# Performance work log

Measured on AMD Instinct MI355X. Metric: run time of the kernel, lower is better.

Reference implementation:

```python
import jax, jax.numpy as jnp
import numpy as np

NUM_HEADS = 16


def setup_inputs() -> dict:
    key = jax.random.key(0)
    ks = jax.random.split(key, 5)
    S, B, N, C = 4, 2, 2048, 1024
    return {
        "x_all": jax.random.normal(ks[0], (S, B, N, C), dtype=jnp.float32),
        "w_qkv": jax.random.normal(ks[1], (C, 3 * C), dtype=jnp.float32) * (C ** -0.5),
        "b_qkv": jax.random.normal(ks[2], (3 * C,), dtype=jnp.float32) * 0.02,
        "w_proj": jax.random.normal(ks[3], (C, C), dtype=jnp.float32) * (C ** -0.5),
        "b_proj": jax.random.normal(ks[4], (C,), dtype=jnp.float32) * 0.02,
    }


def reference(x_all, w_qkv, b_qkv, w_proj, b_proj):
    # x_all: [S, B, N, C] -- S = cp_dim ring shards, each rank holds [B, N, C]
    S, B, N, C = x_all.shape
    H = NUM_HEADS
    D = C // H
    scale = 1.0 / np.sqrt(D).astype(np.float32)

    # same qkv projection on every rank
    qkv = (jnp.einsum("sbnc,ce->sbne", x_all, w_qkv) + b_qkv)
    qkv = qkv.reshape(S, B, N, 3, H, D)
    # rank 0's queries: [B, H, N, D]
    q = jnp.transpose(qkv[0, :, :, 0], (0, 2, 1, 3))
    # all shards' keys/values: [S, B, H, N, D]
    k = jnp.transpose(qkv[:, :, :, 1], (0, 1, 3, 2, 4))
    v = jnp.transpose(qkv[:, :, :, 2], (0, 1, 3, 2, 4))

    # ring loop: online softmax merge across KV shards (numerically stable
    # form of the source's exp(lse)-weighted average)
    attn_out, lse = None, None
    for s in range(S):
        scores = jnp.einsum("bhnd,bhmd->bhnm", q, k[s]) * scale  # [B,H,N,N]
        new_lse = jax.nn.logsumexp(scores, axis=-1)               # [B,H,N]
        probs = jnp.exp(scores - new_lse[..., None])
        new_out = jnp.einsum("bhnm,bhmd->bhnd", probs, v[s])      # [B,H,N,D]
        if attn_out is None:
            attn_out, lse = new_out, new_lse
        else:
            m = jnp.logaddexp(lse, new_lse)
            attn_out = (attn_out * jnp.exp(lse - m)[..., None]
                        + new_out * jnp.exp(new_lse - m)[..., None])
            lse = m

    # [B,H,N,D] -> [B,N,C]
    out = jnp.transpose(attn_out, (0, 2, 1, 3)).reshape(B, N, C)
    return out @ w_proj + b_proj
```

## Files before the change

kernel.cpp:

```cpp
#include <hip/hip_runtime.h>
#include <hip/hip_bf16.h>


typedef __bf16 bf16x8 __attribute__((ext_vector_type(8)));
typedef float v4f __attribute__((ext_vector_type(4)));

#if __has_builtin(__builtin_amdgcn_exp2f)
#define EXP2F(x) __builtin_amdgcn_exp2f(x)
#else
#define EXP2F(x) exp2f(x)
#endif

__device__ __forceinline__ float bf2f(unsigned short h) {
  union { unsigned int u; float f; } a; a.u = ((unsigned int)h) << 16; return a.f;
}
__device__ __forceinline__ unsigned short f2bf(float f) {
  union { float f; unsigned int u; } a; a.f = f;
  unsigned int u = a.u;
  unsigned int r = (u + 0x7fffu + ((u >> 16) & 1u)) >> 16;
  return (unsigned short)r;
}
__device__ __forceinline__ unsigned int pack2t(float a, float b) {
  union { float f; unsigned int u; } ua, ub; ua.f = a; ub.f = b;
#if __has_builtin(__builtin_amdgcn_perm)
  return __builtin_amdgcn_perm(ub.u, ua.u, 0x07060302u);
#else
  return (ua.u >> 16) | (ub.u & 0xffff0000u);
#endif
}
__device__ __forceinline__ bf16x8 ldfrag16(const unsigned short* p) {
  union { uint4 u; bf16x8 v; } x; x.u = *(const uint4*)p; return x.v;
}
__device__ __forceinline__ bf16x8 ones8() {
  union { unsigned short s[8]; bf16x8 v; } x;
#pragma unroll
  for (int i = 0; i < 8; i++) x.s[i] = 0x3F80;
  return x.v;
}
__device__ __forceinline__ void gld_lds16(const unsigned short* g, unsigned short* l) {
  __builtin_amdgcn_global_load_lds((__attribute__((address_space(1))) void*)g,
                                   (__attribute__((address_space(3))) void*)l, 16, 0, 0);
}

__global__ void detect_dtype(const unsigned short* __restrict__ x, int* flag) {
  __shared__ int cnt;
  if (threadIdx.x == 0) cnt = 0;
  __syncthreads();
  int sane = 0;
#pragma unroll
  for (int j = 0; j < 4; j++) {
    unsigned short v = x[2 * (threadIdx.x + 64 * j)];
    int e = (v >> 7) & 0xFF;
    if (e >= 90 && e <= 140) sane++;
  }
  atomicAdd(&cnt, sane);
  __syncthreads();
  if (threadIdx.x == 0) *flag = (cnt > 160) ? 0 : 1;
}

__global__ void conv_to_bf16(const void* __restrict__ in, unsigned short* __restrict__ out,
                             int n4, const int* __restrict__ flag) {
  int i = blockIdx.x * blockDim.x + threadIdx.x;
  if (i >= n4) return;
  if (*flag) {
    float4 v = ((const float4*)in)[i];
    ushort4 o;
    o.x = f2bf(v.x); o.y = f2bf(v.y); o.z = f2bf(v.z); o.w = f2bf(v.w);
    ((ushort4*)out)[i] = o;
  } else {
    ((ushort4*)out)[i] = ((const ushort4*)in)[i];
  }
}

__global__ void conv_bias(const void* __restrict__ bq_in, const void* __restrict__ bp_in,
                          unsigned short* __restrict__ bq, unsigned short* __restrict__ bp,
                          const int* __restrict__ flag) {
  int i = blockIdx.x * 256 + threadIdx.x;
  const void* in = (i < 768) ? bq_in : bp_in;
  unsigned short* out = (i < 768) ? bq : bp;
  int j = (i < 768) ? i : i - 768;
  if (*flag) {
    float4 v = ((const float4*)in)[j];
    ushort4 o;
    o.x = f2bf(v.x); o.y = f2bf(v.y); o.z = f2bf(v.z); o.w = f2bf(v.w);
    ((ushort4*)out)[j] = o;
  } else {
    ((ushort4*)out)[j] = ((const ushort4*)in)[j];
  }
}

__global__ void trans_both(const void* __restrict__ wqkv, const void* __restrict__ wproj,
                           unsigned short* __restrict__ wt1, unsigned short* __restrict__ wt2,
                           const int* __restrict__ flag) {
  __shared__ unsigned short t[32][33];
  int tx = threadIdx.x, ty = threadIdx.y;
  int bx = blockIdx.x;
  const void* in; unsigned short* out; int C, c0;
  if (bx < 96) { in = wqkv; out = wt1; C = 3072; c0 = bx * 32; }
  else         { in = wproj; out = wt2; C = 1024; c0 = (bx - 96) * 32; }
  const int R = 1024;
  int r0 = blockIdx.y * 32;
  int fp = *flag;
#pragma unroll
  for (int j = 0; j < 32; j += 8) {
    unsigned short v;
    if (fp) v = f2bf(((const float*)in)[(r0 + ty + j) * C + c0 + tx]);
    else    v = ((const unsigned short*)in)[(r0 + ty + j) * C + c0 + tx];
    t[ty + j][tx] = v;
  }
  __syncthreads();
#pragma unroll
  for (int j = 0; j < 32; j += 8) out[(c0 + ty + j) * R + r0 + tx] = t[tx][ty + j];
}

template <int MODE>
__launch_bounds__(256, 3)
__global__ void gemm_bt(const unsigned short* __restrict__ A,
                        const unsigned short* __restrict__ Bt,
                        const unsigned short* __restrict__ bias,
                        void* __restrict__ Cout,
                        int K, int ldc, const int* __restrict__ flag,
                        const unsigned short* Bt2, const unsigned short* bias2,
                        void* Cout2,
                        const unsigned short* Bt3, const unsigned short* bias3,
                        void* Cout3) {
  __shared__ unsigned short As[128 * 64];
  __shared__ unsigned short Bs[128 * 64];
  int tid = threadIdx.x;
  int w = tid >> 6, lane = tid & 63, col = lane & 15, quad = lane >> 4;
  int wm = w >> 1, wn = w & 1;
  const unsigned short* Bt_ = Bt;
  const unsigned short* bias_ = bias;
  void* Cout_ = Cout;
  bool isq = false, isv = false;
  int n0, m0;
  if constexpr (MODE == 4) {
    int id = blockIdx.x;
    int xcd = id & 7, t = id >> 3;
    n0 = (t & 7) * 128;
    int y = xcd * 36 + (t >> 3);
    if (y < 256) {
      m0 = (y >> 1) * 128;
      if (y & 1) { isv = true; Bt_ = Bt3; bias_ = bias3; Cout_ = Cout3; }
    } else {
      m0 = (y - 256) * 128;
      isq = true; Bt_ = Bt2; bias_ = bias2; Cout_ = Cout2;
    }
  } else {
    int id = blockIdx.x;
    int xcd = id & 7, t = id >> 3;
    n0 = (t & 7) * 128;
    m0 = (xcd * 4 + (t >> 3)) * 128;
  }
  int fp = 0;
  if constexpr (MODE == 2) fp = *flag;

  v4f acc[4][4];
#pragma unroll
  for (int i = 0; i < 4; i++)
#pragma unroll
    for (int j = 0; j < 4; j++) acc[i][j] = v4f{0.f, 0.f, 0.f, 0.f};

  int row0 = tid >> 3, c0 = tid & 7;
  int sw = c0;
  int cg0 = (sw ^ (row0 & 7)) * 8;
  const unsigned short* ga0 = &A[(m0 + row0) * K + cg0];
  const unsigned short* ga1 = ga0 + 32 * K;
  const unsigned short* ga2 = ga0 + 64 * K;
  const unsigned short* ga3 = ga0 + 96 * K;
  const unsigned short* gb0 = &Bt_[(n0 + row0) * K + cg0];
  const unsigned short* gb1 = gb0 + 32 * K;
  const unsigned short* gb2 = gb0 + 64 * K;
  const unsigned short* gb3 = gb0 + 96 * K;
  unsigned short* lA0 = &As[w * 512];
  unsigned short* lA1 = &As[2048 + w * 512];
  unsigned short* lA2 = &As[4096 + w * 512];
  unsigned short* lA3 = &As[6144 + w * 512];
  unsigned short* lB0 = &Bs[w * 512];
  unsigned short* lB1 = &Bs[2048 + w * 512];
  unsigned short* lB2 = &Bs[4096 + w * 512];
  unsigned short* lB3 = &Bs[6144 + w * 512];

  int niter = K >> 6;
  for (int it = 0; it < niter; it++) {
    __syncthreads();
    gld_lds16(ga0, lA0); gld_lds16(ga1, lA1);
    gld_lds16(ga2, lA2); gld_lds16(ga3, lA3);
    gld_lds16(gb0, lB0); gld_lds16(gb1, lB1);
    gld_lds16(gb2, lB2); gld_lds16(gb3, lB3);
    ga0 += 64; ga1 += 64; ga2 += 64; ga3 += 64;
    gb0 += 64; gb1 += 64; gb2 += 64; gb3 += 64;
    __syncthreads();
#pragma unroll
    for (int kk = 0; kk < 2; kk++) {
      bf16x8 af[4], bfr[4];
#pragma unroll
      for (int mi = 0; mi < 4; mi++) {
        int row = wm * 64 + mi * 16 + col;
        af[mi] = ldfrag16(&As[row * 64 + 8 * ((kk * 4 + quad) ^ (col & 7))]);
      }
#pragma unroll
      for (int ni = 0; ni < 4; ni++) {
        int row = wn * 64 + ni * 16 + col;
        bfr[ni] = ldfrag16(&Bs[row * 64 + 8 * ((kk * 4 + quad) ^ (col & 7))]);
      }
#pragma unroll
      for (int mi = 0; mi < 4; mi++)
#pragma unroll
        for (int ni = 0; ni < 4; ni++)
          acc[mi][ni] = __builtin_amdgcn_mfma_f32_16x16x32_bf16(af[mi], bfr[ni], acc[mi][ni], 0, 0, 0);
    }
  }

  float bv[4];
#pragma unroll
  for (int ni = 0; ni < 4; ni++) bv[ni] = bf2f(bias_[n0 + wn * 64 + ni * 16 + col]);

  if (MODE == 4 && isv) {
    int rgb0 = m0 + wm * 64;
    int s = rgb0 >> 12, b = (rgb0 >> 11) & 1, n = rgb0 & 2047;
    int kvg0 = s * 2048 + n;
#pragma unroll
    for (int ni = 0; ni < 4; ni++) {
      int cg = n0 + wn * 64 + ni * 16 + col;
      int h = cg >> 6, d = cg & 63;
      unsigned short* rowp = &((unsigned short*)Cout_)[((b * 16 + h) * 64 + d) * 8192 + kvg0];
      float bvn = bv[ni];
#pragma unroll
      for (int r = 0; r < 4; r++) {
        ushort2 e, o2;
        e.x = f2bf(acc[0][ni][r] + bvn);
        e.y = f2bf(acc[2][ni][r] + bvn);
        o2.x = f2bf(acc[1][ni][r] + bvn);
        o2.y = f2bf(acc[3][ni][r] + bvn);
        *(ushort2*)&rowp[2 * (quad * 4 + r)] = e;
        *(ushort2*)&rowp[32 + 2 * (quad * 4 + r)] = o2;
      }
    }
  } else {
#pragma unroll
    for (int mi = 0; mi < 4; mi++)
#pragma unroll
      for (int ni = 0; ni < 4; ni++) {
        float vals[4];
#pragma unroll
        for (int r = 0; r < 4; r++) vals[r] = acc[mi][ni][r] + bv[ni];
        if constexpr (MODE == 4) {
          if (isq) {
#pragma unroll
            for (int r = 0; r < 4; r++) vals[r] *= 0.1803368801111601f;
          }
        }
        int rgb = m0 + wm * 64 + mi * 16 + quad * 4;
        int cg  = n0 + wn * 64 + ni * 16 + col;
        if constexpr (MODE == 4) {
          unsigned short* C = (unsigned short*)Cout_;
#pragma unroll
          for (int r = 0; r < 4; r++) C[(rgb + r) * ldc + cg] = f2bf(vals[r]);
        } else {
          if (fp) {
            float* C = (float*)Cout_;
#pragma unroll
            for (int r = 0; r < 4; r++) C[(rgb + r) * ldc + cg] = vals[r];
          } else {
            unsigned short* C = (unsigned short*)Cout_;
#pragma unroll
            for (int r = 0; r < 4; r++) C[(rgb + r) * ldc + cg] = f2bf(vals[r]);
          }
        }
      }
  }
}

__launch_bounds__(512, 4)
__global__ void attn_kernel(const unsigned short* __restrict__ qbuf,
                            const unsigned short* __restrict__ kbuf,
                            const unsigned short* __restrict__ vt,
                            float* __restrict__ po,
                            float* __restrict__ lbuf) {
  __shared__ unsigned short Ks[2][64 * 64];
  __shared__ unsigned short Vs[3][64 * 64];
  int tid = threadIdx.x;
  int w = tid >> 6, lane = tid & 63, col = lane & 15, quad = lane >> 4;
  int id = blockIdx.x;
  int xcd = id & 7, slot = id >> 3;
  int qt = slot & 7, gsub = slot >> 3;
  int g = gsub * 8 + xcd;
  int bh = g >> 1, half = g & 1;
  int b = bh >> 4, h = bh & 15;
  int q0 = qt * 256;

  bf16x8 aQ[2][2];
#pragma unroll
  for (int mj = 0; mj < 2; mj++)
#pragma unroll
    for (int kk = 0; kk < 2; kk++)
      aQ[mj][kk] = ldfrag16(&qbuf[(b * 2048 + q0 + w * 32 + mj * 16 + col) * 1024 +
                                  h * 64 + kk * 32 + quad * 8]);

  int r0 = tid >> 3, c0 = tid & 7;
  const unsigned short* kp = &kbuf[((half * 2) * 4096 + b * 2048 + r0) * 1024 + h * 64 + c0 * 8];
  const unsigned short* vp = &vt[(bh * 64 + r0) * 8192 + half * 4096 + c0 * 8];
  int sdst = r0 * 64 + 8 * (c0 ^ (r0 & 7));

  const bf16x8 vone = ones8();
  v4f o[2][4];
  v4f acc_l[2] = {v4f{0.f, 0.f, 0.f, 0.f}, v4f{0.f, 0.f, 0.f, 0.f}};
#pragma unroll
  for (int mj = 0; mj < 2; mj++)
#pragma unroll
    for (int di = 0; di < 4; di++) o[mj][di] = v4f{0.f, 0.f, 0.f, 0.f};

  {
    uint4 k0 = *(const uint4*)kp, v0 = *(const uint4*)vp;
    *(uint4*)&Ks[0][sdst] = k0;
    *(uint4*)&Vs[0][sdst] = v0;
  }
  kp += 64 * 1024; vp += 64;
  uint4 pk = *(const uint4*)kp, pv = *(const uint4*)vp;
  __syncthreads();

  bf16x8 aP[2][2];
  {
    v4f sc[4][2];
#pragma unroll
    for (int ni = 0; ni < 4; ni++)
#pragma unroll
      for (int mj = 0; mj < 2; mj++) sc[ni][mj] = v4f{0.f, 0.f, 0.f, 0.f};
#pragma unroll
    for (int kk = 0; kk < 2; kk++) {
      bf16x8 aK[4];
#pragma unroll
      for (int ni = 0; ni < 4; ni++) {
        int row = ni * 16 + col;
        aK[ni] = ldfrag16(&Ks[0][row * 64 + 8 * ((kk * 4 + quad) ^ (col & 7))]);
      }
#pragma unroll
      for (int ni = 0; ni < 4; ni++)
#pragma unroll
        for (int mj = 0; mj < 2; mj++)
          sc[ni][mj] = __builtin_amdgcn_mfma_f32_16x16x32_bf16(aK[ni], aQ[mj][kk], sc[ni][mj], 0, 0, 0);
    }
#pragma unroll
    for (int ni = 0; ni < 4; ni++)
#pragma unroll
      for (int mj = 0; mj < 2; mj++)
#pragma unroll
        for (int r = 0; r < 4; r++) sc[ni][mj][r] = EXP2F(sc[ni][mj][r]);
#pragma unroll
    for (int mj = 0; mj < 2; mj++)
#pragma unroll
      for (int kk = 0; kk < 2; kk++) {
        union { unsigned int d[4]; bf16x8 v; } u;
#pragma unroll
        for (int t = 0; t < 4; t++)
          u.d[t] = pack2t(sc[kk][mj][t], sc[kk + 2][mj][t]);
        aP[mj][kk] = u.v;
      }
  }
  *(uint4*)&Ks[1][sdst] = pk;
  *(uint4*)&Vs[1][sdst] = pv;
  __syncthreads();

  const unsigned short* vprev = Vs[0];
  const unsigned short* vcur  = Vs[1];
  const unsigned short* vnext = Vs[2];

  for (int t = 1; t < 64; t++) {
    const unsigned short* kcur = Ks[t & 1];
    unsigned short* knxt = (unsigned short*)Ks[(t + 1) & 1];
    if (t < 63) {
      int kstep = (((t + 1) & 31) == 0) ? (2048 + 64) * 1024 : 64 * 1024;
      kp += kstep; vp += 64;
      pk = *(const uint4*)kp; pv = *(const uint4*)vp;
    }

    v4f sc[4][2];
#pragma unroll
    for (int ni = 0; ni < 4; ni++)
#pragma unroll
      for (int mj = 0; mj < 2; mj++) sc[ni][mj] = v4f{0.f, 0.f, 0.f, 0.f};
#pragma unroll
    for (int kk = 0; kk < 2; kk++) {
      bf16x8 aK[4];
#pragma unroll
      for (int ni = 0; ni < 4; ni++) {
        int row = ni * 16 + col;
        aK[ni] = ldfrag16(&kcur[row * 64 + 8 * ((kk * 4 + quad) ^ (col & 7))]);
      }
#pragma unroll
      for (int ni = 0; ni < 4; ni++)
#pragma unroll
        for (int mj = 0; mj < 2; mj++)
          sc[ni][mj] = __builtin_amdgcn_mfma_f32_16x16x32_bf16(aK[ni], aQ[mj][kk], sc[ni][mj], 0, 0, 0);
    }

#pragma unroll
    for (int kk = 0; kk < 2; kk++) {
#pragma unroll
      for (int mj = 0; mj < 2; mj++)
        acc_l[mj] = __builtin_amdgcn_mfma_f32_16x16x32_bf16(aP[mj][kk], vone, acc_l[mj], 0, 0, 0);
      bf16x8 bV[4];
#pragma unroll
      for (int di = 0; di < 4; di++) {
        int row = di * 16 + col;
        bV[di] = ldfrag16(&vprev[row * 64 + 8 * ((kk * 4 + quad) ^ (col & 7))]);
      }
#pragma unroll
      for (int mj = 0; mj < 2; mj++)
#pragma unroll
        for (int di = 0; di < 4; di++)
          o[mj][di] = __builtin_amdgcn_mfma_f32_16x16x32_bf16(aP[mj][kk], bV[di], o[mj][di], 0, 0, 0);
    }

#pragma unroll
    for (int ni = 0; ni < 4; ni++)
#pragma unroll
      for (int mj = 0; mj < 2; mj++)
#pragma unroll
        for (int r = 0; r < 4; r++) sc[ni][mj][r] = EXP2F(sc[ni][mj][r]);
    bf16x8 aPn[2][2];
#pragma unroll
    for (int mj = 0; mj < 2; mj++)
#pragma unroll
      for (int kk = 0; kk < 2; kk++) {
        union { unsigned int d[4]; bf16x8 v; } u;
#pragma unroll
        for (int tt = 0; tt < 4; tt++)
          u.d[tt] = pack2t(sc[kk][mj][tt], sc[kk + 2][mj][tt]);
        aPn[mj][kk] = u.v;
      }

    if (t < 63) {
      *(uint4*)&knxt[sdst] = pk;
      *(uint4*)&((unsigned short*)vnext)[sdst] = pv;
    }

    __syncthreads();

#pragma unroll
    for (int mj = 0; mj < 2; mj++)
#pragma unroll
      for (int kk = 0; kk < 2; kk++) aP[mj][kk] = aPn[mj][kk];
    const unsigned short* vt_ = vprev;
    vprev = vcur; vcur = vnext; vnext = vt_;
  }

#pragma unroll
  for (int kk = 0; kk < 2; kk++) {
#pragma unroll
    for (int mj = 0; mj < 2; mj++)
      acc_l[mj] = __builtin_amdgcn_mfma_f32_16x16x32_bf16(aP[mj][kk], vone, acc_l[mj], 0, 0, 0);
    bf16x8 bV[4];
#pragma unroll
    for (int di = 0; di < 4; di++) {
      int row = di * 16 + col;
      bV[di] = ldfrag16(&vprev[row * 64 + 8 * ((kk * 4 + quad) ^ (col & 7))]);
    }
#pragma unroll
    for (int mj = 0; mj < 2; mj++)
#pragma unroll
      for (int di = 0; di < 4; di++)
        o[mj][di] = __builtin_amdgcn_mfma_f32_16x16x32_bf16(aP[mj][kk], bV[di], o[mj][di], 0, 0, 0);
  }

  float* pb = po + half * 4194304;
#pragma unroll
  for (int mj = 0; mj < 2; mj++)
#pragma unroll
    for (int r = 0; r < 4; r++) {
      int n = q0 + w * 32 + mj * 16 + quad * 4 + r;
      if (col == 0) lbuf[half * 65536 + (b * 16 + h) * 2048 + n] = acc_l[mj][r];
#pragma unroll
      for (int di = 0; di < 4; di++) {
        int c = h * 64 + di * 16 + col;
        pb[(b * 2048 + n) * 1024 + c] = o[mj][di][r];
      }
    }
}

__global__ void merge_halves(const float* __restrict__ po, const float* __restrict__ lbuf,
                             unsigned short* __restrict__ attn) {
  int i = blockIdx.x * 256 + threadIdx.x;
  int r = i >> 8, c4 = i & 255;
  float l = lbuf[((r >> 11) * 16 + (c4 >> 4)) * 2048 + (r & 2047)] +
            lbuf[65536 + ((r >> 11) * 16 + (c4 >> 4)) * 2048 + (r & 2047)];
  float inv = 1.f / l;
  float4 a = ((const float4*)po)[i];
  float4 b = ((const float4*)po)[1048576 + i];
  ushort4 o;
  o.x = f2bf((a.x + b.x) * inv); o.y = f2bf((a.y + b.y) * inv);
  o.z = f2bf((a.z + b.z) * inv); o.w = f2bf((a.w + b.w) * inv);
  ((ushort4*)attn)[i] = o;
}

extern "C" void kernel_launch(void* const* d_in, const int* in_sizes, int n_in,
                              void* d_out, int out_size, void* d_ws, size_t ws_size,
                              hipStream_t stream) {
  const void* x      = d_in[0];
  const void* w_qkv  = d_in[1];
  const void* b_qkv  = d_in[2];
  const void* w_proj = d_in[3];
  const void* b_proj = d_in[4];

  char* ws = (char*)d_ws;
  unsigned short* xb   = (unsigned short*)(ws);
  unsigned short* kk   = (unsigned short*)(ws + 33554432);
  unsigned short* vt   = (unsigned short*)(ws + 67108864);
  unsigned short* q0b  = (unsigned short*)(ws + 100663296);
  unsigned short* attn = (unsigned short*)(ws + 109051904);
  unsigned short* wt1  = (unsigned short*)(ws + 117440512);
  unsigned short* wt2  = (unsigned short*)(ws + 123731968);
  unsigned short* bq   = (unsigned short*)(ws + 125829120);
  unsigned short* bp   = (unsigned short*)(ws + 125835264);
  int* flag            = (int*)(ws + 125837312);
  float* po   = (float*)xb;
  float* lbuf = (float*)wt1;

  detect_dtype<<<1, 64, 0, stream>>>((const unsigned short*)x, flag);

  conv_to_bf16<<<16384, 256, 0, stream>>>(x, xb, 4194304, flag);
  conv_bias<<<4, 256, 0, stream>>>(b_qkv, b_proj, bq, bp, flag);
  trans_both<<<dim3(128, 32), dim3(32, 8), 0, stream>>>(w_qkv, w_proj, wt1, wt2, flag);

  gemm_bt<4><<<2304, 256, 0, stream>>>(xb, wt1 + 1024 * 1024, bq + 1024, kk,
                                       1024, 1024, flag,
                                       wt1, bq, q0b,
                                       wt1 + 2048 * 1024, bq + 2048, vt);

  attn_kernel<<<512, 512, 0, stream>>>(q0b, kk, vt, po, lbuf);
  merge_halves<<<4096, 256, 0, stream>>>(po, lbuf, attn);

  gemm_bt<2><<<256, 256, 0, stream>>>(attn, wt2, bp, d_out,
                                      1024, 1024, flag,
                                      nullptr, nullptr, nullptr,
                                      nullptr, nullptr, nullptr);
}
```

Before: 265.4 us.

## Fuse fp32-to-bf16 input conversion into QKV GEMM A-tile loading

Removes the standalone kernel that converted x to bf16 in workspace and instead has the QKV GEMM load fp32 x directly, convert in registers, and write bf16 into LDS with a one-iteration register prefetch. This eliminates a full read/write pass over the input and the re-read of the bf16 copy. In exchange the GEMM reads twice as many bytes per A tile, repeated across column tiles, and loses the asynchronous global-to-LDS path for A.

Result: slower. 300.9 us (+13.4%).

```diff
diff --git a/kernel.cpp b/kernel.cpp
--- a/kernel.cpp
+++ b/kernel.cpp
@@ -28,6 +28,12 @@
   return (ua.u >> 16) | (ub.u & 0xffff0000u);
 #endif
 }
+__device__ __forceinline__ uint4 cvt8(float4 a, float4 b) {
+  union { unsigned short s[8]; uint4 u; } r;
+  r.s[0] = f2bf(a.x); r.s[1] = f2bf(a.y); r.s[2] = f2bf(a.z); r.s[3] = f2bf(a.w);
+  r.s[4] = f2bf(b.x); r.s[5] = f2bf(b.y); r.s[6] = f2bf(b.z); r.s[7] = f2bf(b.w);
+  return r.u;
+}
 __device__ __forceinline__ bf16x8 ldfrag16(const unsigned short* p) {
   union { uint4 u; bf16x8 v; } x; x.u = *(const uint4*)p; return x.v;
 }
@@ -56,20 +62,6 @@
   atomicAdd(&cnt, sane);
   __syncthreads();
   if (threadIdx.x == 0) *flag = (cnt > 160) ? 0 : 1;
-}
-
-__global__ void conv_to_bf16(const void* __restrict__ in, unsigned short* __restrict__ out,
-                             int n4, const int* __restrict__ flag) {
-  int i = blockIdx.x * blockDim.x + threadIdx.x;
-  if (i >= n4) return;
-  if (*flag) {
-    float4 v = ((const float4*)in)[i];
-    ushort4 o;
-    o.x = f2bf(v.x); o.y = f2bf(v.y); o.z = f2bf(v.z); o.w = f2bf(v.w);
-    ((ushort4*)out)[i] = o;
-  } else {
-    ((ushort4*)out)[i] = ((const ushort4*)in)[i];
-  }
 }
 
 __global__ void conv_bias(const void* __restrict__ bq_in, const void* __restrict__ bp_in,
@@ -153,7 +145,7 @@
     m0 = (xcd * 4 + (t >> 3)) * 128;
   }
   int fp = 0;
-  if constexpr (MODE == 2) fp = *flag;
+  if constexpr (MODE == 2 || MODE == 4) fp = *flag;
 
   v4f acc[4][4];
 #pragma unroll
@@ -162,34 +154,68 @@
     for (int j = 0; j < 4; j++) acc[i][j] = v4f{0.f, 0.f, 0.f, 0.f};
 
   int row0 = tid >> 3, c0 = tid & 7;
-  int sw = c0;
-  int cg0 = (sw ^ (row0 & 7)) * 8;
-  const unsigned short* ga0 = &A[(m0 + row0) * K + cg0];
+  int csw = (c0 ^ (row0 & 7)) * 8;
+  const unsigned short* gb0 = &Bt_[(n0 + row0) * K + csw];
+  const unsigned short* gb1 = gb0 + 32 * K;
+  const unsigned short* gb2 = gb0 + 64 * K;
+  const unsigned short* gb3 = gb0 + 96 * K;
+  unsigned short* lB0 = &Bs[w * 512];
+  unsigned short* lB1 = &Bs[2048 + w * 512];
+  unsigned short* lB2 = &Bs[4096 + w * 512];
+  unsigned short* lB3 = &Bs[6144 + w * 512];
+
+  const unsigned short* ga0 = &A[(m0 + row0) * K + csw];
   const unsigned short* ga1 = ga0 + 32 * K;
   const unsigned short* ga2 = ga0 + 64 * K;
   const unsigned short* ga3 = ga0 + 96 * K;
-  const unsigned short* gb0 = &Bt_[(n0 + row0) * K + cg0];
-  const unsigned short* gb1 = gb0 + 32 * K;
-  const unsigned short* gb2 = gb0 + 64 * K;
-  const unsigned short* gb3 = gb0 + 96 * K;
   unsigned short* lA0 = &As[w * 512];
   unsigned short* lA1 = &As[2048 + w * 512];
   unsigned short* lA2 = &As[4096 + w * 512];
   unsigned short* lA3 = &As[6144 + w * 512];
-  unsigned short* lB0 = &Bs[w * 512];
-  unsigned short* lB1 = &Bs[2048 + w * 512];
-  unsigned short* lB2 = &Bs[4096 + w * 512];
-  unsigned short* lB3 = &Bs[6144 + w * 512];
+  const float* pf0 = (const float*)A + (m0 + row0) * K + csw;
+  const float* pf1 = pf0 + 32 * K;
+  const float* pf2 = pf0 + 64 * K;
+  const float* pf3 = pf0 + 96 * K;
+  unsigned short* dA0 = &As[row0 * 64 + c0 * 8];
+  unsigned short* dA1 = dA0 + 32 * 64;
+  unsigned short* dA2 = dA0 + 64 * 64;
+  unsigned short* dA3 = dA0 + 96 * 64;
+  uint4 wA0, wA1, wA2, wA3;
+
+#define LOADA(IT)                                                              \
+  if (fp) {                                                                    \
+    const float* q0_ = pf0 + (IT) * 64; const float* q1_ = pf1 + (IT) * 64;    \
+    const float* q2_ = pf2 + (IT) * 64; const float* q3_ = pf3 + (IT) * 64;    \
+    wA0 = cvt8(*(const float4*)q0_, *(const float4*)(q0_ + 4));                \
+    wA1 = cvt8(*(const float4*)q1_, *(const float4*)(q1_ + 4));                \
+    wA2 = cvt8(*(const float4*)q2_, *(const float4*)(q2_ + 4));                \
+    wA3 = cvt8(*(const float4*)q3_, *(const float4*)(q3_ + 4));                \
+  } else {                                                                     \
+    wA0 = *(const uint4*)(ga0 + (IT) * 64);                                    \
+    wA1 = *(const uint4*)(ga1 + (IT) * 64);                                    \
+    wA2 = *(const uint4*)(ga2 + (IT) * 64);                                    \
+    wA3 = *(const uint4*)(ga3 + (IT) * 64);                                    \
+  }
 
   int niter = K >> 6;
+  if constexpr (MODE == 4) { LOADA(0); }
   for (int it = 0; it < niter; it++) {
     __syncthreads();
-    gld_lds16(ga0, lA0); gld_lds16(ga1, lA1);
-    gld_lds16(ga2, lA2); gld_lds16(ga3, lA3);
-    gld_lds16(gb0, lB0); gld_lds16(gb1, lB1);
-    gld_lds16(gb2, lB2); gld_lds16(gb3, lB3);
-    ga0 += 64; ga1 += 64; ga2 += 64; ga3 += 64;
-    gb0 += 64; gb1 += 64; gb2 += 64; gb3 += 64;
+    if constexpr (MODE == 4) {
+      *(uint4*)dA0 = wA0; *(uint4*)dA1 = wA1;
+      *(uint4*)dA2 = wA2; *(uint4*)dA3 = wA3;
+      gld_lds16(gb0, lB0); gld_lds16(gb1, lB1);
+      gld_lds16(gb2, lB2); gld_lds16(gb3, lB3);
+      gb0 += 64; gb1 += 64; gb2 += 64; gb3 += 64;
+      if (it + 1 < niter) { LOADA(it + 1); }
+    } else {
+      gld_lds16(ga0, lA0); gld_lds16(ga1, lA1);
+      gld_lds16(ga2, lA2); gld_lds16(ga3, lA3);
+      gld_lds16(gb0, lB0); gld_lds16(gb1, lB1);
+      gld_lds16(gb2, lB2); gld_lds16(gb3, lB3);
+      ga0 += 64; ga1 += 64; ga2 += 64; ga3 += 64;
+      gb0 += 64; gb1 += 64; gb2 += 64; gb3 += 64;
+    }
     __syncthreads();
 #pragma unroll
     for (int kk = 0; kk < 2; kk++) {
@@ -211,6 +237,7 @@
           acc[mi][ni] = __builtin_amdgcn_mfma_f32_16x16x32_bf16(af[mi], bfr[ni], acc[mi][ni], 0, 0, 0);
     }
   }
+#undef LOADA
 
   float bv[4];
 #pragma unroll
@@ -504,7 +531,6 @@
   const void* b_proj = d_in[4];
 
   char* ws = (char*)d_ws;
-  unsigned short* xb   = (unsigned short*)(ws);
   unsigned short* kk   = (unsigned short*)(ws + 33554432);
   unsigned short* vt   = (unsigned short*)(ws + 67108864);
   unsigned short* q0b  = (unsigned short*)(ws + 100663296);
@@ -514,16 +540,16 @@
   unsigned short* bq   = (unsigned short*)(ws + 125829120);
   unsigned short* bp   = (unsigned short*)(ws + 125835264);
   int* flag            = (int*)(ws + 125837312);
-  float* po   = (float*)xb;
+  float* po   = (float*)ws;
   float* lbuf = (float*)wt1;
 
   detect_dtype<<<1, 64, 0, stream>>>((const unsigned short*)x, flag);
 
-  conv_to_bf16<<<16384, 256, 0, stream>>>(x, xb, 4194304, flag);
   conv_bias<<<4, 256, 0, stream>>>(b_qkv, b_proj, bq, bp, flag);
   trans_both<<<dim3(128, 32), dim3(32, 8), 0, stream>>>(w_qkv, w_proj, wt1, wt2, flag);
 
-  gemm_bt<4><<<2304, 256, 0, stream>>>(xb, wt1 + 1024 * 1024, bq + 1024, kk,
+  gemm_bt<4><<<2304, 256, 0, stream>>>((const unsigned short*)x,
+                                       wt1 + 1024 * 1024, bq + 1024, kk,
                                        1024, 1024, flag,
                                        wt1, bq, q0b,
                                        wt1 + 2048 * 1024, bq + 2048, vt);
```
